# Performance work log

Hardware: AMD Instinct MI355X
Metric: run time of the kernel (lower is better)

## Reference

```python
import jax, jax.numpy as jnp
import numpy as np

N_DIM = 512
HEADS = 8
NUM_EXPERTS = 65536
NUM_KEYS = 256      # sqrt(NUM_EXPERTS)
DIM_KEY = 256       # N_DIM // 2
TOPK = 16           # num_experts_per_head (also product_key_topk)
SCALE = 0.02


def setup_inputs() -> dict:
    key = jax.random.key(0)
    k0, k1, k2, k3, k4 = jax.random.split(key, 5)
    x = jax.random.normal(k0, (1, 2048, N_DIM), dtype=jnp.float32)
    W_q = jax.random.normal(k1, (N_DIM, 2 * HEADS * DIM_KEY), dtype=jnp.float32) * SCALE
    keys = jax.random.normal(k2, (HEADS, NUM_KEYS, 2, DIM_KEY), dtype=jnp.float32) * SCALE
    down_embed = jax.random.normal(k3, (NUM_EXPERTS, N_DIM), dtype=jnp.float32) * SCALE
    up_embed = jax.random.normal(k4, (NUM_EXPERTS, N_DIM), dtype=jnp.float32) * SCALE
    return {"x": x, "W_q": W_q, "keys": keys, "down_embed": down_embed, "up_embed": up_embed}


def reference(x, W_q, keys, down_embed, up_embed):
    b, n, d = x.shape
    # queries: [b,n,2*h*dk] -> [2,b,n,h,dk]
    q = (x @ W_q).reshape(b, n, 2, HEADS, DIM_KEY).transpose(2, 0, 1, 3, 4)
    # similarity against product keys: [2,b,n,h,num_keys]
    sim = jnp.einsum('pbnhd,hkpd->pbnhk', q, keys)
    sx, ix = jax.lax.top_k(sim[0], TOPK)   # [b,n,h,TOPK]
    sy, iy = jax.lax.top_k(sim[1], TOPK)
    # cartesian product of the two top-k sets -> [b,n,h,TOPK*TOPK]
    all_scores = (sx[..., :, None] + sy[..., None, :]).reshape(b, n, HEADS, TOPK * TOPK)
    scores, pk_idx = jax.lax.top_k(all_scores, TOPK)  # [b,n,h,TOPK]
    # NOTE: original module indexes embeddings with pk_idx (flat top-k positions),
    # reproduced faithfully here.
    w_down = down_embed[pk_idx]  # [b,n,h,TOPK,d]
    w_up = up_embed[pk_idx]      # [b,n,h,TOPK,d]
    h = jnp.einsum('bnd,bnhkd->bnhk', x, w_down)
    h = jax.nn.gelu(h, approximate=False)
    h = jax.nn.softmax(scores, axis=-1) * h
    return jnp.einsum('bnhk,bnhkd->bnd', h, w_up)
```

## Files before the change

### kernel.cpp

```cpp
#include <hip/hip_runtime.h>
#include <math.h>

#define N_TOK 2048
#define NDIM 512
#define HEADS 8
#define TOPK 16
#define QCOLS 4096
#define MCOLS 4352

typedef __attribute__((ext_vector_type(8))) _Float16 f16x8;
typedef __attribute__((ext_vector_type(4))) float f32x4;

__device__ __forceinline__ unsigned short f32_to_f16(float f) {
    _Float16 h = (_Float16)f;
    return __builtin_bit_cast(unsigned short, h);
}
__device__ __forceinline__ float f16_to_f32(unsigned short u) {
    return (float)__builtin_bit_cast(_Float16, u);
}
__device__ __forceinline__ void gl_lds16(const void* g, void* l) {
    __builtin_amdgcn_global_load_lds(
        (const __attribute__((address_space(1))) void*)g,
        (__attribute__((address_space(3))) void*)l, 16, 0, 0);
}

__global__ __launch_bounds__(256) void kPrep(const float* __restrict__ x,
                                             const float* __restrict__ down,
                                             unsigned short* __restrict__ xh,
                                             unsigned short* __restrict__ xl,
                                             unsigned short* __restrict__ Mth,
                                             unsigned short* __restrict__ Mtl) {
    const int bid = blockIdx.x;
    const int tid = threadIdx.x;
    if (bid < 1024) {
        const int i = bid * 256 + tid;
        float4 v = reinterpret_cast<const float4*>(x)[i];
        float vv[4] = {v.x, v.y, v.z, v.w};
        ushort4 h, lo;
        unsigned short* hp = &h.x; unsigned short* lp = &lo.x;
        #pragma unroll
        for (int t = 0; t < 4; ++t) {
            unsigned short hh = f32_to_f16(vv[t]);
            hp[t] = hh;
            lp[t] = f32_to_f16(vv[t] - f16_to_f32(hh));
        }
        reinterpret_cast<ushort4*>(xh)[i] = h;
        reinterpret_cast<ushort4*>(xl)[i] = lo;
    } else {
        const int e = bid - 1024;
        const int d0 = tid * 2;
        float2 v = *reinterpret_cast<const float2*>(&down[(size_t)e * NDIM + d0]);
        ushort2 h, lo;
        unsigned short h0 = f32_to_f16(v.x);
        unsigned short h1 = f32_to_f16(v.y);
        h.x = h0; h.y = h1;
        lo.x = f32_to_f16(v.x - f16_to_f32(h0));
        lo.y = f32_to_f16(v.y - f16_to_f32(h1));
        *reinterpret_cast<ushort2*>(&Mth[(size_t)(QCOLS + e) * NDIM + d0]) = h;
        *reinterpret_cast<ushort2*>(&Mtl[(size_t)(QCOLS + e) * NDIM + d0]) = lo;
    }
}

__global__ __launch_bounds__(256) void k1_combine(const float* __restrict__ Wq,
                                                  const float* __restrict__ keys,
                                                  unsigned short* __restrict__ Mth,
                                                  unsigned short* __restrict__ Mtl) {
    __shared__ float As[16][64];
    __shared__ float Bs[16][64];
    const int ph = blockIdx.z;
    const int p = ph >> 3, h = ph & 7;
    const int off = p * 2048 + h * 256;
    const int c0 = blockIdx.x * 64;
    const int k0 = blockIdx.y * 64;
    const int tid = threadIdx.x;
    const int lr = tid >> 2;
    const int ld4 = (tid & 3) * 4;
    const int tr = tid >> 4, tc = tid & 15;
    float acc[4][4] = {};
    const float* ap = &Wq[(size_t)(c0 + lr) * QCOLS + off + ld4];
    const float* bp = &keys[(size_t)((h * 256 + (k0 + lr)) * 2 + p) * 256 + ld4];
    float4 av = *reinterpret_cast<const float4*>(ap);
    float4 bv = *reinterpret_cast<const float4*>(bp);
    for (int d0 = 0; d0 < 256; d0 += 16) {
        __syncthreads();
        As[ld4 + 0][lr] = av.x; As[ld4 + 1][lr] = av.y; As[ld4 + 2][lr] = av.z; As[ld4 + 3][lr] = av.w;
        Bs[ld4 + 0][lr] = bv.x; Bs[ld4 + 1][lr] = bv.y; Bs[ld4 + 2][lr] = bv.z; Bs[ld4 + 3][lr] = bv.w;
        __syncthreads();
        if (d0 + 16 < 256) {
            av = *reinterpret_cast<const float4*>(ap + d0 + 16);
            bv = *reinterpret_cast<const float4*>(bp + d0 + 16);
        }
        #pragma unroll
        for (int kk = 0; kk < 16; ++kk) {
            float4 a = *reinterpret_cast<const float4*>(&As[kk][tr * 4]);
            float4 b = *reinterpret_cast<const float4*>(&Bs[kk][tc * 4]);
            float aa[4] = {a.x, a.y, a.z, a.w}, bb[4] = {b.x, b.y, b.z, b.w};
            #pragma unroll
            for (int i = 0; i < 4; ++i)
                #pragma unroll
                for (int j = 0; j < 4; ++j) acc[i][j] += aa[i] * bb[j];
        }
    }
    #pragma unroll
    for (int j = 0; j < 4; ++j) {
        const int col = off + k0 + tc * 4 + j;
        ushort4 h4, l4;
        unsigned short* hp = &h4.x; unsigned short* lp = &l4.x;
        #pragma unroll
        for (int i = 0; i < 4; ++i) {
            float v = acc[i][j];
            unsigned short hh = f32_to_f16(v);
            hp[i] = hh;
            lp[i] = f32_to_f16(v - f16_to_f32(hh));
        }
        *reinterpret_cast<ushort4*>(&Mth[(size_t)col * NDIM + c0 + tr * 4]) = h4;
        *reinterpret_cast<ushort4*>(&Mtl[(size_t)col * NDIM + c0 + tr * 4]) = l4;
    }
}

#define BM 64
#define BN 128
#define BK 32
#define ABYTES 8192
#define BBYTES 16384
#define BUFBYTES 24576
__global__ __launch_bounds__(256, 3) void k2_mfma(const unsigned short* __restrict__ xh,
                                                  const unsigned short* __restrict__ xl,
                                                  const unsigned short* __restrict__ Mth,
                                                  const unsigned short* __restrict__ Mtl,
                                                  float* __restrict__ C) {
    __shared__ __align__(16) char lds[2 * BUFBYTES];
    const int tid = threadIdx.x;
    const int w = tid >> 6, l = tid & 63;
    const int row0 = blockIdx.x * BM;
    const int col0 = blockIdx.y * BN;
    const int wm = w >> 1, wn = w & 1;
    f32x4 acc[2][4] = {};

    auto stage = [&](int buf, int s) {
        const int kk = s * BK;
        char* base = lds + buf * BUFBYTES;
        #pragma unroll
        for (int t = 0; t < 2; ++t) {
            const int q = w * 2048 + t * 1024 + l * 16;
            const int r = q >> 7;
            const int bsw = (q & 127) ^ ((r & 7) << 4);
            const unsigned short* src = (bsw < 64)
                ? xh + (size_t)(row0 + r) * NDIM + kk + (bsw >> 1)
                : xl + (size_t)(row0 + r) * NDIM + kk + ((bsw - 64) >> 1);
            gl_lds16(src, base + w * 2048 + t * 1024);
        }
        #pragma unroll
        for (int t = 0; t < 4; ++t) {
            const int q = w * 4096 + t * 1024 + l * 16;
            const int r = q >> 7;
            const int bsw = (q & 127) ^ ((r & 7) << 4);
            const unsigned short* src = (bsw < 64)
                ? Mth + (size_t)(col0 + r) * NDIM + kk + (bsw >> 1)
                : Mtl + (size_t)(col0 + r) * NDIM + kk + ((bsw - 64) >> 1);
            gl_lds16(src, base + ABYTES + w * 4096 + t * 1024);
        }
    };

    stage(0, 0);
    __syncthreads();
    for (int s = 0; s < 16; ++s) {
        if (s + 1 < 16) stage((s + 1) & 1, s + 1);
        const char* base = lds + (s & 1) * BUFBYTES;
        const int bq = (l >> 4) * 16;
        f16x8 ah[2], al[2], bh[4], bl[4];
        #pragma unroll
        for (int mi = 0; mi < 2; ++mi) {
            const int ra = wm * 32 + mi * 16 + (l & 15);
            const int swz = (ra & 7) << 4;
            ah[mi] = *(const f16x8*)(base + ra * 128 + (bq ^ swz));
            al[mi] = *(const f16x8*)(base + ra * 128 + ((bq + 64) ^ swz));
        }
        #pragma unroll
        for (int nj = 0; nj < 4; ++nj) {
            const int rb = wn * 64 + nj * 16 + (l & 15);
            const int swz = (rb & 7) << 4;
            bh[nj] = *(const f16x8*)(base + ABYTES + rb * 128 + (bq ^ swz));
            bl[nj] = *(const f16x8*)(base + ABYTES + rb * 128 + ((bq + 64) ^ swz));
        }
        #pragma unroll
        for (int mi = 0; mi < 2; ++mi)
            #pragma unroll
            for (int nj = 0; nj < 4; ++nj) {
                acc[mi][nj] = __builtin_amdgcn_mfma_f32_16x16x32_f16(ah[mi], bh[nj], acc[mi][nj], 0, 0, 0);
                acc[mi][nj] = __builtin_amdgcn_mfma_f32_16x16x32_f16(ah[mi], bl[nj], acc[mi][nj], 0, 0, 0);
                acc[mi][nj] = __builtin_amdgcn_mfma_f32_16x16x32_f16(al[mi], bh[nj], acc[mi][nj], 0, 0, 0);
            }
        __syncthreads();
    }
    #pragma unroll
    for (int mi = 0; mi < 2; ++mi)
        #pragma unroll
        for (int nj = 0; nj < 4; ++nj)
            #pragma unroll
            for (int r = 0; r < 4; ++r) {
                const int row = row0 + wm * 32 + mi * 16 + (l >> 4) * 4 + r;
                const int col = col0 + wn * 64 + nj * 16 + (l & 15);
                C[(size_t)row * MCOLS + col] = acc[mi][nj][r];
            }
}

__device__ const unsigned short CAND_TBL[32] = {
    0x0100, 0x0302, 0x0504, 0x0706, 0x0908, 0x0B0A, 0x0D0C, 0x0F0E,
    0x1110, 0x1312, 0x1514, 0x1716,
    0x2120, 0x2322, 0x3024, 0x3231, 0x4033, 0x4241,
    0x5150, 0x6160, 0x7170,
    0x9080, 0xB0A0, 0xD0C0, 0xF0E0,
    0xFFFF, 0xFFFF, 0xFFFF, 0xFFFF, 0xFFFF, 0xFFFF, 0xFFFF
};

__device__ __forceinline__ float sel16(const float a[16], int i) {
    float b0 = (i & 1) ? a[1] : a[0];
    float b1 = (i & 1) ? a[3] : a[2];
    float b2 = (i & 1) ? a[5] : a[4];
    float b3 = (i & 1) ? a[7] : a[6];
    float b4 = (i & 1) ? a[9] : a[8];
    float b5 = (i & 1) ? a[11] : a[10];
    float b6 = (i & 1) ? a[13] : a[12];
    float b7 = (i & 1) ? a[15] : a[14];
    float c0 = (i & 2) ? b1 : b0;
    float c1 = (i & 2) ? b3 : b2;
    float c2 = (i & 2) ? b5 : b4;
    float c3 = (i & 2) ? b7 : b6;
    float d0 = (i & 4) ? c1 : c0;
    float d1 = (i & 4) ? c3 : c2;
    return (i & 8) ? d1 : d0;
}

__global__ __launch_bounds__(256) void k3_sel(const float* __restrict__ sim,
                                              float* __restrict__ W) {
    __shared__ unsigned long long ckey[8][50];
    __shared__ float winval[8][16];
    __shared__ int winflat[8][16];
    __shared__ int Wrow[256];

    const int tid = threadIdx.x;
    const int n = blockIdx.x;
    const int h = tid >> 5;
    const int lam = tid & 15;
    const int p = (tid >> 4) & 1;

    Wrow[tid] = 0;

    const float* s = sim + (size_t)n * MCOLS + p * 2048 + h * 256 + lam * 16;
    float v[16];
    #pragma unroll
    for (int c = 0; c < 4; ++c) {
        float4 t = *reinterpret_cast<const float4*>(s + c * 4);
        v[c * 4 + 0] = t.x; v[c * 4 + 1] = t.y; v[c * 4 + 2] = t.z; v[c * 4 + 3] = t.w;
    }

    #pragma unroll
    for (int k = 2; k <= 16; k <<= 1)
        #pragma unroll
        for (int j = k >> 1; j > 0; j >>= 1)
            #pragma unroll
            for (int i = 0; i < 16; ++i) {
                const int l2 = i ^ j;
                if (l2 > i) {
                    const bool asc = ((i & k) == 0);
                    const float lo = fminf(v[i], v[l2]), hi = fmaxf(v[i], v[l2]);
                    v[i] = asc ? lo : hi;
                    v[l2] = asc ? hi : lo;
                }
            }

    #pragma unroll
    for (int lvl = 1; lvl <= 8; lvl <<= 1) {
        float m[16];
        #pragma unroll
        for (int q = 0; q < 16; ++q)
            m[q] = fmaxf(v[q], __shfl_xor(v[15 - q], lvl));
        #pragma unroll
        for (int j = 8; j > 0; j >>= 1)
            #pragma unroll
            for (int i = 0; i < 16; ++i) {
                const int l2 = i ^ j;
                if (l2 > i) {
                    const float lo = fminf(m[i], m[l2]), hi = fmaxf(m[i], m[l2]);
                    m[i] = lo; m[l2] = hi;
                }
            }
        #pragma unroll
        for (int q = 0; q < 16; ++q) v[q] = m[q];
    }

    float other[16];
    #pragma unroll
    for (int q = 0; q < 16; ++q) other[q] = __shfl_xor(v[q], 16);
    const bool isP1 = (tid & 16) != 0;
    float sxd[16], syd[16];
    #pragma unroll
    for (int q = 0; q < 16; ++q) {
        const float own = v[15 - q], oth = other[15 - q];
        sxd[q] = isP1 ? oth : own;
        syd[q] = isP1 ? own : oth;
    }

    const int lc = tid & 31;
    const unsigned int cw = CAND_TBL[lc];
    unsigned long long mykey[2]; float myval[2]; int myflat[2]; int myrank[2] = {0, 0};
    #pragma unroll
    for (int u = 0; u < 2; ++u) {
        const int fl = (cw >> (8 * u)) & 0xFF;
        const float sv = sel16(sxd, fl >> 4) + sel16(syd, fl & 15);
        const unsigned int uv = __float_as_uint(sv);
        const unsigned int mo = (uv & 0x80000000u) ? ~uv : (uv | 0x80000000u);
        mykey[u] = ((unsigned long long)mo << 8) | (unsigned long long)(255 - fl);
        myval[u] = sv; myflat[u] = fl;
        const int slot = lc * 2 + u;
        if (slot < 50) ckey[h][slot] = mykey[u];
    }
    __syncthreads();
    for (int kk = 0; kk < 50; ++kk) {
        const unsigned long long ok = ckey[h][kk];
        myrank[0] += (ok > mykey[0]) ? 1 : 0;
        myrank[1] += (ok > mykey[1]) ? 1 : 0;
    }
    #pragma unroll
    for (int u = 0; u < 2; ++u)
        if (myrank[u] < 16) { winval[h][myrank[u]] = myval[u]; winflat[h][myrank[u]] = myflat[u]; }
    __syncthreads();

    if (!(tid & 16)) {
        const float sc = winval[h][lam];
        const float m0 = winval[h][0];
        float e = expf(sc - m0);
        float esum = e;
        #pragma unroll
        for (int off = 1; off < 16; off <<= 1) esum += __shfl_xor(esum, off);
        const int fl = winflat[h][lam];
        const float hv = sim[(size_t)n * MCOLS + QCOLS + fl];
        const float g = 0.5f * hv * (1.0f + erff(hv * 0.70710678118654752f));
        const float w = (e / esum) * g;
        atomicAdd(&Wrow[fl], __float2int_rn(w * 4194304.0f));
    }
    __syncthreads();
    W[(size_t)n * 256 + tid] = (float)Wrow[tid] * (1.0f / 4194304.0f);
}

__global__ __launch_bounds__(256) void k5_out(const float* __restrict__ W,
                                              const float* __restrict__ up,
                                              float* __restrict__ out) {
    __shared__ float As[16][32];
    __shared__ float Bs[16][64];
    const int row0 = blockIdx.x * 32;
    const int col0 = blockIdx.y * 64;
    const int tid = threadIdx.x;
    const int ar = tid & 31, ak = (tid >> 5) * 2;
    const int bk = tid >> 4, bc = (tid & 15) * 4;
    const int r0 = (tid >> 4) * 2, c0 = (tid & 15) * 4;
    float acc[2][4] = {};
    const float* wp = &W[(size_t)(row0 + ar) * 256 + ak];
    const float* up0 = &up[(size_t)bk * NDIM + col0 + bc];
    float2 a2 = *reinterpret_cast<const float2*>(wp);
    float4 b4 = *reinterpret_cast<const float4*>(up0);
    for (int k0 = 0; k0 < 256; k0 += 16) {
        __syncthreads();
        As[ak + 0][ar] = a2.x;
        As[ak + 1][ar] = a2.y;
        *reinterpret_cast<float4*>(&Bs[bk][bc]) = b4;
        __syncthreads();
        if (k0 + 16 < 256) {
            a2 = *reinterpret_cast<const float2*>(wp + k0 + 16);
            b4 = *reinterpret_cast<const float4*>(up0 + (size_t)16 * NDIM + (size_t)k0 * NDIM);
        }
        #pragma unroll
        for (int kk = 0; kk < 16; ++kk) {
            const float a0 = As[kk][r0], a1 = As[kk][r0 + 1];
            float4 b = *reinterpret_cast<const float4*>(&Bs[kk][c0]);
            float bb[4] = {b.x, b.y, b.z, b.w};
            #pragma unroll
            for (int j = 0; j < 4; ++j) {
                acc[0][j] += a0 * bb[j];
                acc[1][j] += a1 * bb[j];
            }
        }
    }
    #pragma unroll
    for (int i = 0; i < 2; ++i) {
        float4 o = {acc[i][0], acc[i][1], acc[i][2], acc[i][3]};
        *reinterpret_cast<float4*>(&out[(size_t)(row0 + r0 + i) * NDIM + col0 + c0]) = o;
    }
}

extern "C" void kernel_launch(void* const* d_in, const int* in_sizes, int n_in,
                              void* d_out, int out_size, void* d_ws, size_t ws_size,
                              hipStream_t stream) {
    const float* x    = (const float*)d_in[0];
    const float* Wq   = (const float*)d_in[1];
    const float* keys = (const float*)d_in[2];
    const float* down = (const float*)d_in[3];
    const float* up   = (const float*)d_in[4];
    float* out = (float*)d_out;

    char* ws = (char*)d_ws;
    unsigned short* Mth = (unsigned short*)(ws);
    unsigned short* Mtl = (unsigned short*)(ws + 4456448);
    unsigned short* xh  = (unsigned short*)(ws + 8912896);
    unsigned short* xl  = (unsigned short*)(ws + 11010048);
    float* sim          = (float*)(ws + 13107200);
    float* W            = (float*)(ws + 48758784);

    kPrep<<<1280, 256, 0, stream>>>(x, down, xh, xl, Mth, Mtl);
    k1_combine<<<dim3(8, 4, 16), 256, 0, stream>>>(Wq, keys, Mth, Mtl);
    k2_mfma<<<dim3(32, 34), 256, 0, stream>>>(xh, xl, Mth, Mtl, sim);
    k3_sel<<<2048, 256, 0, stream>>>(sim, W);
    k5_out<<<dim3(64, 8), 256, 0, stream>>>(W, up, out);
}
```

Baseline: 105.2 us.

## Fuse per-head top-k into GEMM epilogue and merge prep kernels

The GEMM now uses 64x256 tiles so that each block covers one full head-half of 256 key scores. In its epilogue it stages the tile in LDS, runs the bitonic top-16 selection there, and writes only 16 sorted scores per row plus the down-projection column block. This removes the large float sim matrix round trip and most of the selection work from the combine kernel. The prep and query-key combine kernels are merged into one launch, and s_setprio is set around the MFMA loop. The bigger tile raises LDS use and register pressure (occupancy hint drops from 3 to 2 waves per SIMD), and the grid shrinks to 544 blocks.

```diff
diff --git a/kernel.cpp b/kernel.cpp
--- a/kernel.cpp
+++ b/kernel.cpp
@@ -6,7 +6,6 @@
 #define HEADS 8
 #define TOPK 16
 #define QCOLS 4096
-#define MCOLS 4352
 
 typedef __attribute__((ext_vector_type(8))) _Float16 f16x8;
 typedef __attribute__((ext_vector_type(4))) float f32x4;
@@ -24,30 +23,37 @@
         (__attribute__((address_space(3))) void*)l, 16, 0, 0);
 }
 
-__global__ __launch_bounds__(256) void kPrep(const float* __restrict__ x,
-                                             const float* __restrict__ down,
-                                             unsigned short* __restrict__ xh,
-                                             unsigned short* __restrict__ xl,
-                                             unsigned short* __restrict__ Mth,
-                                             unsigned short* __restrict__ Mtl) {
+__global__ __launch_bounds__(256) void k0_prep(const float* __restrict__ x,
+                                               const float* __restrict__ down,
+                                               const float* __restrict__ Wq,
+                                               const float* __restrict__ keys,
+                                               unsigned short* __restrict__ xh,
+                                               unsigned short* __restrict__ xl,
+                                               unsigned short* __restrict__ Mth,
+                                               unsigned short* __restrict__ Mtl) {
     const int bid = blockIdx.x;
     const int tid = threadIdx.x;
-    if (bid < 1024) {
-        const int i = bid * 256 + tid;
-        float4 v = reinterpret_cast<const float4*>(x)[i];
-        float vv[4] = {v.x, v.y, v.z, v.w};
-        ushort4 h, lo;
-        unsigned short* hp = &h.x; unsigned short* lp = &lo.x;
+    if (bid < 256) {
         #pragma unroll
         for (int t = 0; t < 4; ++t) {
-            unsigned short hh = f32_to_f16(vv[t]);
-            hp[t] = hh;
-            lp[t] = f32_to_f16(vv[t] - f16_to_f32(hh));
-        }
-        reinterpret_cast<ushort4*>(xh)[i] = h;
-        reinterpret_cast<ushort4*>(xl)[i] = lo;
-    } else {
-        const int e = bid - 1024;
+            const int i = bid * 1024 + t * 256 + tid;
+            float4 v = reinterpret_cast<const float4*>(x)[i];
+            float vv[4] = {v.x, v.y, v.z, v.w};
+            ushort4 h, lo;
+            unsigned short* hp = &h.x; unsigned short* lp = &lo.x;
+            #pragma unroll
+            for (int q = 0; q < 4; ++q) {
+                unsigned short hh = f32_to_f16(vv[q]);
+                hp[q] = hh;
+                lp[q] = f32_to_f16(vv[q] - f16_to_f32(hh));
+            }
+            reinterpret_cast<ushort4*>(xh)[i] = h;
+            reinterpret_cast<ushort4*>(xl)[i] = lo;
+        }
+        return;
+    }
+    if (bid < 512) {
+        const int e = bid - 256;
         const int d0 = tid * 2;
         float2 v = *reinterpret_cast<const float2*>(&down[(size_t)e * NDIM + d0]);
         ushort2 h, lo;
@@ -58,21 +64,16 @@
         lo.y = f32_to_f16(v.y - f16_to_f32(h1));
         *reinterpret_cast<ushort2*>(&Mth[(size_t)(QCOLS + e) * NDIM + d0]) = h;
         *reinterpret_cast<ushort2*>(&Mtl[(size_t)(QCOLS + e) * NDIM + d0]) = lo;
-    }
-}
-
-__global__ __launch_bounds__(256) void k1_combine(const float* __restrict__ Wq,
-                                                  const float* __restrict__ keys,
-                                                  unsigned short* __restrict__ Mth,
-                                                  unsigned short* __restrict__ Mtl) {
+        return;
+    }
     __shared__ float As[16][64];
     __shared__ float Bs[16][64];
-    const int ph = blockIdx.z;
+    const int b = bid - 512;
+    const int cx = b & 7, ky = (b >> 3) & 3, ph = b >> 5;
     const int p = ph >> 3, h = ph & 7;
     const int off = p * 2048 + h * 256;
-    const int c0 = blockIdx.x * 64;
-    const int k0 = blockIdx.y * 64;
-    const int tid = threadIdx.x;
+    const int c0 = cx * 64;
+    const int k0 = ky * 64;
     const int lr = tid >> 2;
     const int ld4 = (tid & 3) * 4;
     const int tr = tid >> 4, tc = tid & 15;
@@ -93,8 +94,8 @@
         #pragma unroll
         for (int kk = 0; kk < 16; ++kk) {
             float4 a = *reinterpret_cast<const float4*>(&As[kk][tr * 4]);
-            float4 b = *reinterpret_cast<const float4*>(&Bs[kk][tc * 4]);
-            float aa[4] = {a.x, a.y, a.z, a.w}, bb[4] = {b.x, b.y, b.z, b.w};
+            float4 bq = *reinterpret_cast<const float4*>(&Bs[kk][tc * 4]);
+            float aa[4] = {a.x, a.y, a.z, a.w}, bb[4] = {bq.x, bq.y, bq.z, bq.w};
             #pragma unroll
             for (int i = 0; i < 4; ++i)
                 #pragma unroll
@@ -119,27 +120,26 @@
 }
 
 #define BM 64
-#define BN 128
+#define BN 256
 #define BK 32
-#define ABYTES 8192
-#define BBYTES 16384
-#define BUFBYTES 24576
-__global__ __launch_bounds__(256, 3) void k2_mfma(const unsigned short* __restrict__ xh,
+#define FBUF 40960
+__global__ __launch_bounds__(256, 2) void kF_gemm(const unsigned short* __restrict__ xh,
                                                   const unsigned short* __restrict__ xl,
                                                   const unsigned short* __restrict__ Mth,
                                                   const unsigned short* __restrict__ Mtl,
-                                                  float* __restrict__ C) {
-    __shared__ __align__(16) char lds[2 * BUFBYTES];
+                                                  float* __restrict__ T,
+                                                  float* __restrict__ D) {
+    __shared__ __align__(16) char lds[2 * FBUF];
     const int tid = threadIdx.x;
     const int w = tid >> 6, l = tid & 63;
     const int row0 = blockIdx.x * BM;
-    const int col0 = blockIdx.y * BN;
-    const int wm = w >> 1, wn = w & 1;
-    f32x4 acc[2][4] = {};
+    const int g = blockIdx.y;
+    const int colbase = g * 256;
+    f32x4 acc[4][4] = {};
 
     auto stage = [&](int buf, int s) {
         const int kk = s * BK;
-        char* base = lds + buf * BUFBYTES;
+        char* base = lds + buf * FBUF;
         #pragma unroll
         for (int t = 0; t < 2; ++t) {
             const int q = w * 2048 + t * 1024 + l * 16;
@@ -151,14 +151,14 @@
             gl_lds16(src, base + w * 2048 + t * 1024);
         }
         #pragma unroll
-        for (int t = 0; t < 4; ++t) {
-            const int q = w * 4096 + t * 1024 + l * 16;
+        for (int t = 0; t < 8; ++t) {
+            const int q = w * 8192 + t * 1024 + l * 16;
             const int r = q >> 7;
             const int bsw = (q & 127) ^ ((r & 7) << 4);
             const unsigned short* src = (bsw < 64)
-                ? Mth + (size_t)(col0 + r) * NDIM + kk + (bsw >> 1)
-                : Mtl + (size_t)(col0 + r) * NDIM + kk + ((bsw - 64) >> 1);
-            gl_lds16(src, base + ABYTES + w * 4096 + t * 1024);
+                ? Mth + (size_t)(colbase + r) * NDIM + kk + (bsw >> 1)
+                : Mtl + (size_t)(colbase + r) * NDIM + kk + ((bsw - 64) >> 1);
+            gl_lds16(src, base + 8192 + w * 8192 + t * 1024);
         }
     };
 
@@ -166,43 +166,105 @@
     __syncthreads();
     for (int s = 0; s < 16; ++s) {
         if (s + 1 < 16) stage((s + 1) & 1, s + 1);
-        const char* base = lds + (s & 1) * BUFBYTES;
+        const char* base = lds + (s & 1) * FBUF;
         const int bq = (l >> 4) * 16;
-        f16x8 ah[2], al[2], bh[4], bl[4];
-        #pragma unroll
-        for (int mi = 0; mi < 2; ++mi) {
-            const int ra = wm * 32 + mi * 16 + (l & 15);
+        f16x8 ah[4], al[4], bh[4], bl[4];
+        #pragma unroll
+        for (int mi = 0; mi < 4; ++mi) {
+            const int ra = mi * 16 + (l & 15);
             const int swz = (ra & 7) << 4;
             ah[mi] = *(const f16x8*)(base + ra * 128 + (bq ^ swz));
             al[mi] = *(const f16x8*)(base + ra * 128 + ((bq + 64) ^ swz));
         }
         #pragma unroll
         for (int nj = 0; nj < 4; ++nj) {
-            const int rb = wn * 64 + nj * 16 + (l & 15);
+            const int rb = w * 64 + nj * 16 + (l & 15);
             const int swz = (rb & 7) << 4;
-            bh[nj] = *(const f16x8*)(base + ABYTES + rb * 128 + (bq ^ swz));
-            bl[nj] = *(const f16x8*)(base + ABYTES + rb * 128 + ((bq + 64) ^ swz));
-        }
-        #pragma unroll
-        for (int mi = 0; mi < 2; ++mi)
+            bh[nj] = *(const f16x8*)(base + 8192 + rb * 128 + (bq ^ swz));
+            bl[nj] = *(const f16x8*)(base + 8192 + rb * 128 + ((bq + 64) ^ swz));
+        }
+        __builtin_amdgcn_s_setprio(1);
+        #pragma unroll
+        for (int mi = 0; mi < 4; ++mi)
             #pragma unroll
             for (int nj = 0; nj < 4; ++nj) {
                 acc[mi][nj] = __builtin_amdgcn_mfma_f32_16x16x32_f16(ah[mi], bh[nj], acc[mi][nj], 0, 0, 0);
                 acc[mi][nj] = __builtin_amdgcn_mfma_f32_16x16x32_f16(ah[mi], bl[nj], acc[mi][nj], 0, 0, 0);
                 acc[mi][nj] = __builtin_amdgcn_mfma_f32_16x16x32_f16(al[mi], bh[nj], acc[mi][nj], 0, 0, 0);
             }
+        __builtin_amdgcn_s_setprio(0);
         __syncthreads();
     }
-    #pragma unroll
-    for (int mi = 0; mi < 2; ++mi)
+
+    if (g == 16) {
+        #pragma unroll
+        for (int mi = 0; mi < 4; ++mi)
+            #pragma unroll
+            for (int nj = 0; nj < 4; ++nj)
+                #pragma unroll
+                for (int r = 0; r < 4; ++r) {
+                    const int row = row0 + mi * 16 + (l >> 4) * 4 + r;
+                    const int col = w * 64 + nj * 16 + (l & 15);
+                    D[(size_t)row * 256 + col] = acc[mi][nj][r];
+                }
+        return;
+    }
+
+    float* Cl = (float*)lds;
+    #pragma unroll
+    for (int mi = 0; mi < 4; ++mi)
         #pragma unroll
         for (int nj = 0; nj < 4; ++nj)
             #pragma unroll
-            for (int r = 0; r < 4; ++r) {
-                const int row = row0 + wm * 32 + mi * 16 + (l >> 4) * 4 + r;
-                const int col = col0 + wn * 64 + nj * 16 + (l & 15);
-                C[(size_t)row * MCOLS + col] = acc[mi][nj][r];
-            }
+            for (int r = 0; r < 4; ++r)
+                Cl[(mi * 16 + (l >> 4) * 4 + r) * 260 + w * 64 + nj * 16 + (l & 15)] = acc[mi][nj][r];
+    __syncthreads();
+
+    const int grp = tid >> 4;
+    const int lam = tid & 15;
+    #pragma unroll
+    for (int rr = 0; rr < 4; ++rr) {
+        const int row = grp * 4 + rr;
+        float v[16];
+        #pragma unroll
+        for (int j = 0; j < 16; ++j) v[j] = Cl[row * 260 + lam + 16 * j];
+
+        #pragma unroll
+        for (int k = 2; k <= 16; k <<= 1)
+            #pragma unroll
+            for (int j = k >> 1; j > 0; j >>= 1)
+                #pragma unroll
+                for (int i = 0; i < 16; ++i) {
+                    const int l2 = i ^ j;
+                    if (l2 > i) {
+                        const bool asc = ((i & k) == 0);
+                        const float lo = fminf(v[i], v[l2]), hi = fmaxf(v[i], v[l2]);
+                        v[i] = asc ? lo : hi;
+                        v[l2] = asc ? hi : lo;
+                    }
+                }
+        #pragma unroll
+        for (int lvl = 1; lvl <= 8; lvl <<= 1) {
+            float m[16];
+            #pragma unroll
+            for (int q = 0; q < 16; ++q)
+                m[q] = fmaxf(v[q], __shfl_xor(v[15 - q], lvl));
+            #pragma unroll
+            for (int j = 8; j > 0; j >>= 1)
+                #pragma unroll
+                for (int i = 0; i < 16; ++i) {
+                    const int l2 = i ^ j;
+                    if (l2 > i) {
+                        const float lo = fminf(m[i], m[l2]), hi = fmaxf(m[i], m[l2]);
+                        m[i] = lo; m[l2] = hi;
+                    }
+                }
+            #pragma unroll
+            for (int q = 0; q < 16; ++q) v[q] = m[q];
+        }
+        const int n = row0 + row;
+        T[((size_t)n * 16 + g) * 16 + lam] = v[15 - lam];
+    }
 }
 
 __device__ const unsigned short CAND_TBL[32] = {
@@ -232,8 +294,9 @@
     return (i & 8) ? d1 : d0;
 }
 
-__global__ __launch_bounds__(256) void k3_sel(const float* __restrict__ sim,
-                                              float* __restrict__ W) {
+__global__ __launch_bounds__(256) void kC_combine(const float* __restrict__ T,
+                                                  const float* __restrict__ D,
+                                                  float* __restrict__ W) {
     __shared__ unsigned long long ckey[8][50];
     __shared__ float winval[8][16];
     __shared__ int winflat[8][16];
@@ -243,64 +306,14 @@
     const int n = blockIdx.x;
     const int h = tid >> 5;
     const int lam = tid & 15;
-    const int p = (tid >> 4) & 1;
 
     Wrow[tid] = 0;
 
-    const float* s = sim + (size_t)n * MCOLS + p * 2048 + h * 256 + lam * 16;
-    float v[16];
-    #pragma unroll
-    for (int c = 0; c < 4; ++c) {
-        float4 t = *reinterpret_cast<const float4*>(s + c * 4);
-        v[c * 4 + 0] = t.x; v[c * 4 + 1] = t.y; v[c * 4 + 2] = t.z; v[c * 4 + 3] = t.w;
-    }
-
-    #pragma unroll
-    for (int k = 2; k <= 16; k <<= 1)
-        #pragma unroll
-        for (int j = k >> 1; j > 0; j >>= 1)
-            #pragma unroll
-            for (int i = 0; i < 16; ++i) {
-                const int l2 = i ^ j;
-                if (l2 > i) {
-                    const bool asc = ((i & k) == 0);
-                    const float lo = fminf(v[i], v[l2]), hi = fmaxf(v[i], v[l2]);
-                    v[i] = asc ? lo : hi;
-                    v[l2] = asc ? hi : lo;
-                }
-            }
-
-    #pragma unroll
-    for (int lvl = 1; lvl <= 8; lvl <<= 1) {
-        float m[16];
-        #pragma unroll
-        for (int q = 0; q < 16; ++q)
-            m[q] = fmaxf(v[q], __shfl_xor(v[15 - q], lvl));
-        #pragma unroll
-        for (int j = 8; j > 0; j >>= 1)
-            #pragma unroll
-            for (int i = 0; i < 16; ++i) {
-                const int l2 = i ^ j;
-                if (l2 > i) {
-                    const float lo = fminf(m[i], m[l2]), hi = fmaxf(m[i], m[l2]);
-                    m[i] = lo; m[l2] = hi;
-                }
-            }
-        #pragma unroll
-        for (int q = 0; q < 16; ++q) v[q] = m[q];
-    }
-
-    float other[16];
-    #pragma unroll
-    for (int q = 0; q < 16; ++q) other[q] = __shfl_xor(v[q], 16);
-    const bool isP1 = (tid & 16) != 0;
     float sxd[16], syd[16];
-    #pragma unroll
-    for (int q = 0; q < 16; ++q) {
-        const float own = v[15 - q], oth = other[15 - q];
-        sxd[q] = isP1 ? oth : own;
-        syd[q] = isP1 ? own : oth;
-    }
+    const float* t0 = &T[((size_t)n * 16 + h) * 16];
+    const float* t1 = &T[((size_t)n * 16 + 8 + h) * 16];
+    #pragma unroll
+    for (int q = 0; q < 16; ++q) { sxd[q] = t0[q]; syd[q] = t1[q]; }
 
     const int lc = tid & 31;
     const unsigned int cw = CAND_TBL[lc];
@@ -335,10 +348,10 @@
         #pragma unroll
         for (int off = 1; off < 16; off <<= 1) esum += __shfl_xor(esum, off);
         const int fl = winflat[h][lam];
-        const float hv = sim[(size_t)n * MCOLS + QCOLS + fl];
-        const float g = 0.5f * hv * (1.0f + erff(hv * 0.70710678118654752f));
-        const float w = (e / esum) * g;
-        atomicAdd(&Wrow[fl], __float2int_rn(w * 4194304.0f));
+        const float hv = D[(size_t)n * 256 + fl];
+        const float gg = 0.5f * hv * (1.0f + erff(hv * 0.70710678118654752f));
+        const float wv = (e / esum) * gg;
+        atomicAdd(&Wrow[fl], __float2int_rn(wv * 4194304.0f));
     }
     __syncthreads();
     W[(size_t)n * 256 + tid] = (float)Wrow[tid] * (1.0f / 4194304.0f);
@@ -404,12 +417,12 @@
     unsigned short* Mtl = (unsigned short*)(ws + 4456448);
     unsigned short* xh  = (unsigned short*)(ws + 8912896);
     unsigned short* xl  = (unsigned short*)(ws + 11010048);
-    float* sim          = (float*)(ws + 13107200);
-    float* W            = (float*)(ws + 48758784);
-
-    kPrep<<<1280, 256, 0, stream>>>(x, down, xh, xl, Mth, Mtl);
-    k1_combine<<<dim3(8, 4, 16), 256, 0, stream>>>(Wq, keys, Mth, Mtl);
-    k2_mfma<<<dim3(32, 34), 256, 0, stream>>>(xh, xl, Mth, Mtl, sim);
-    k3_sel<<<2048, 256, 0, stream>>>(sim, W);
+    float* T            = (float*)(ws + 13107200);
+    float* D            = (float*)(ws + 15204352);
+    float* W            = (float*)(ws + 17301504);
+
+    k0_prep<<<1024, 256, 0, stream>>>(x, down, Wq, keys, xh, xl, Mth, Mtl);
+    kF_gemm<<<dim3(32, 17), 256, 0, stream>>>(xh, xl, Mth, Mtl, T, D);
+    kC_combine<<<2048, 256, 0, stream>>>(T, D, W);
     k5_out<<<dim3(64, 8), 256, 0, stream>>>(W, up, out);
 }
```

After: 101.9 us. -3.2%, faster.
